# Kernel optimization log

Hardware: AMD Instinct MI355X
Metric: run time of the kernel (lower is better)

The kernel has to match this reference:

```python
import jax, jax.numpy as jnp
import numpy as np

B, T, C = 4, 2048, 768
H, N = 12, 64
N_LAYER, LAYER_ID = 12, 1
EPS_GN = 0.00064


def setup_inputs():
    key = jax.random.key(0)
    ks = jax.random.split(key, 20)
    r01 = LAYER_ID / (N_LAYER - 1)
    r10 = 1.0 - LAYER_ID / N_LAYER
    ddd = (np.arange(C, dtype=np.float64) / C)[None, None, :]

    def lam(p, off=0.0):
        return jnp.asarray(1.0 - np.power(ddd, p) - off, dtype=jnp.float32)

    decay = -7.0 + 5.0 * (np.arange(C, dtype=np.float64) / (C - 1)) ** (0.85 + r01 ** 0.5)

    def rn(i, shape, scale):
        return scale * jax.random.normal(ks[i], shape, jnp.float32)

    s = 1.0 / C ** 0.5
    return {
        "x": jax.random.normal(ks[0], (B, T, C), jnp.float32),
        "v_first": jax.random.normal(ks[1], (B, T, C), jnp.float32),
        "lambda_r": lam(0.2 * r10), "lambda_w": lam(0.9 * r10),
        "lambda_k": lam(0.9 * r10, 0.4 * r01), "lambda_v": lam(0.4 * r10, 0.6 * r01),
        "lambda_a": lam(0.9 * r10), "lambda_g": lam(0.2 * r10),
        "w_miu": jnp.asarray(decay[None, None, :] + 0.5, jnp.float32),
        "w_A": rn(2, (C, 64), 0.02), "w_B": rn(3, (64, C), 0.02),
        "a_miu": jnp.zeros((1, 1, C), jnp.float32),
        "a_A": rn(4, (C, 64), 0.02), "a_B": rn(5, (64, C), 0.02),
        "v_miu": jnp.ones((1, 1, C), jnp.float32),
        "v_A": rn(6, (C, 64), 0.02), "v_B": rn(7, (64, C), 0.02),
        "g_A": rn(8, (C, 128), 0.02), "g_B": rn(9, (128, C), 0.02),
        "k_k": 0.85 * jnp.ones((1, 1, C), jnp.float32),
        "k_a": jnp.ones((1, 1, C), jnp.float32),
        "r_k": rn(10, (H, N), 0.02),
        "W_r": jax.random.uniform(ks[11], (C, C), jnp.float32, -0.5 * s, 0.5 * s),
        "W_k": jax.random.uniform(ks[12], (C, C), jnp.float32, -0.05 * s, 0.05 * s),
        "W_v": jax.random.uniform(ks[13], (C, C), jnp.float32, -0.5 * s, 0.5 * s),
        "W_o": rn(14, (C, C), 0.02),
        "ln_w": jnp.ones((C,), jnp.float32), "ln_b": jnp.zeros((C,), jnp.float32),
    }


def _wkv7(r, w, k, v, z, b):
    # r,w,k,v,z,b: (B,T,H,N). RWKV-7 linear recurrence with per-head NxN state:
    # S_t = S_{t-1}*diag(exp(-exp(w_t))) + (S_{t-1} z_t) b_t^T + v_t k_t^T ; y_t = S_t r_t
    decay = jnp.exp(-jnp.exp(w))

    def step(S, inp):
        rt, dt, kt, vt, zt, bt = inp  # each (B,H,N)
        sa = jnp.einsum('bhij,bhj->bhi', S, zt)
        S = S * dt[:, :, None, :] + sa[..., None] * bt[:, :, None, :] + vt[..., None] * kt[:, :, None, :]
        y = jnp.einsum('bhij,bhj->bhi', S, rt)
        return S, y

    seq = tuple(jnp.moveaxis(t, 1, 0) for t in (r, decay, k, v, z, b))  # (T,B,H,N)
    S0 = jnp.zeros((r.shape[0], r.shape[2], r.shape[3], r.shape[3]), r.dtype)
    _, ys = jax.lax.scan(step, S0, seq)
    return jnp.moveaxis(ys, 0, 1)  # (B,T,H,N)


def reference(x, v_first, lambda_r, lambda_w, lambda_k, lambda_v, lambda_a, lambda_g,
              w_miu, w_A, w_B, a_miu, a_A, a_B, v_miu, v_A, v_B, g_A, g_B,
              k_k, k_a, r_k, W_r, W_k, W_v, W_o, ln_w, ln_b):
    Bb, Tt, Cc = x.shape
    # ZeroPad2d((0,0,1,-1)): shift sequence right by 1, zero at t=0
    x_shift = jnp.pad(x, ((0, 0), (1, 0), (0, 0)))[:, :-1]
    xd = x_shift - x
    r = (x + xd * lambda_r) @ W_r.T
    w = x + xd * lambda_w
    k = (x + xd * lambda_k) @ W_k.T
    v = (x + xd * lambda_v) @ W_v.T
    a_in = x + xd * lambda_a
    g_in = x + xd * lambda_g
    if LAYER_ID == 0:
        v_first = v
    else:
        v = v + (v_first - v) * jax.nn.sigmoid(v_miu + (v @ v_A) @ v_B)
    w = -jax.nn.softplus(-(w_miu + jnp.tanh(w @ w_A) @ w_B)) - 0.5
    a = jax.nn.sigmoid(a_miu + (a_in @ a_A) @ a_B)
    g = jax.nn.sigmoid(g_in @ g_A) @ g_B
    kk = (k * k_k).reshape(Bb, Tt, H, N)
    kk = kk / jnp.maximum(jnp.linalg.norm(kk, axis=-1, keepdims=True), 1e-12)
    k = k * (1 + (a - 1) * k_a)
    rh = r.reshape(Bb, Tt, H, N)
    wh = w.reshape(Bb, Tt, H, N)
    kh = k.reshape(Bb, Tt, H, N)
    vh = v.reshape(Bb, Tt, H, N)
    ah = a.reshape(Bb, Tt, H, N)
    y = _wkv7(rh, wh, kh, vh, -kk, kk * ah)  # (B,T,H,N)
    # GroupNorm over heads, eps=0.00064, biased variance (torch semantics)
    mu = y.mean(-1, keepdims=True)
    var = y.var(-1, keepdims=True)
    y = ((y - mu) / jnp.sqrt(var + EPS_GN)).reshape(Bb, Tt, Cc) * ln_w + ln_b
    y = y + ((rh * kh * r_k).sum(-1, keepdims=True) * vh).reshape(Bb, Tt, Cc)
    out = (y * g) @ W_o.T
    return (out, v_first)
```

## Files before the change

### kernel.cpp

```cpp
#include <hip/hip_runtime.h>
#include <hip/hip_bf16.h>
#include <math.h>


#define B_  4
#define T_  2048
#define C_  768
#define H_  12

typedef __attribute__((ext_vector_type(8))) short bf16x8;
typedef __attribute__((ext_vector_type(4))) float f32x4;

#define GLD16(gsrc, ldst)                                                     \
  __builtin_amdgcn_global_load_lds(                                           \
      (const __attribute__((address_space(1))) void*)(gsrc),                  \
      (__attribute__((address_space(3))) void*)(ldst), 16, 0, 0)

template <int CTRL>
static __device__ __forceinline__ float row_ror_add(float v) {
  int t = __builtin_amdgcn_update_dpp(0, __float_as_int(v), CTRL, 0xF, 0xF, true);
  return v + __int_as_float(t);
}
static __device__ __forceinline__ float row_sum16(float v) {
  v = row_ror_add<0x128>(v);
  v = row_ror_add<0x124>(v);
  v = row_ror_add<0x122>(v);
  v = row_ror_add<0x121>(v);
  return v;
}

static __device__ __forceinline__ float wave_sum64(float v) {
  v = row_sum16(v);
  v += __shfl_xor(v, 16);
  v += __shfl_xor(v, 32);
  return v;
}

static __device__ __forceinline__ short bf16b(float f) {
  __hip_bfloat16 h = __float2bfloat16(f);
  return *reinterpret_cast<short*>(&h);
}

enum { EPI_NONE = 0, EPI_TANH, EPI_WDECAY, EPI_SIGBIAS, EPI_SIGMOID, EPI_VMIX };

static __device__ __forceinline__ float apply_epi_f(int epi, float val, int n,
                                                    int gmrow, int N,
                                                    const float* bias,
                                                    const float* ex1,
                                                    const float* ex2) {
  if (epi == EPI_TANH) {
    val = tanhf(val);
  } else if (epi == EPI_WDECAY) {
    const float u = bias[n] + val;
    const float sig = 1.f / (1.f + expf(-u));
    val = expf(-0.60653065971263342f * sig);
  } else if (epi == EPI_SIGBIAS) {
    const float u = bias[n] + val;
    val = 1.f / (1.f + expf(-u));
  } else if (epi == EPI_SIGMOID) {
    val = 1.f / (1.f + expf(-val));
  } else if (epi == EPI_VMIX) {
    const float u = bias[n] + val;
    const float sg = 1.f / (1.f + expf(-u));
    const size_t off = (size_t)gmrow * N + n;
    const float v0v = ex1[off];
    const float vf = ex2[off];
    val = v0v + (vf - v0v) * sg;
  }
  return val;
}

static __device__ __forceinline__ void gemm128_tile(
    const short* __restrict__ A, const short* __restrict__ Bw,
    float* __restrict__ C, short* __restrict__ C16, int M, int N, int K,
    int bx, int by, int epi, const float* bias, const float* ex1,
    const float* ex2, short* As, short* Bs) {
  const int tid = threadIdx.x;
  const int wave = tid >> 6, lane = tid & 63;
  const int m0 = by * 128, n0 = bx * 128;
  const int wm = (wave >> 1) * 64, wn = (wave & 1) * 64;
  const int fr = lane & 15, fk = (lane >> 4) * 8;

  f32x4 acc[4][4];
#pragma unroll
  for (int i = 0; i < 4; i++)
#pragma unroll
    for (int j = 0; j < 4; j++) acc[i][j] = (f32x4){0.f, 0.f, 0.f, 0.f};

  const int srow = tid >> 2, scol = (tid & 3) * 8;
  const short* gA = A + (size_t)(m0 + srow) * K + scol;
  const short* gB = Bw + (size_t)(n0 + srow) * K + scol;
  short* lA0 = &As[wave * 512];
  short* lA1 = &As[2048 + wave * 512];
  short* lB0 = &Bs[wave * 512];
  short* lB1 = &Bs[2048 + wave * 512];

  for (int k0 = 0; k0 < K; k0 += 32) {
    GLD16(gA + k0, lA0);
    GLD16(gA + (size_t)64 * K + k0, lA1);
    GLD16(gB + k0, lB0);
    GLD16(gB + (size_t)64 * K + k0, lB1);
    __syncthreads();

    bf16x8 af[4], bf[4];
#pragma unroll
    for (int i = 0; i < 4; i++)
      af[i] = *(const bf16x8*)&As[(wm + i * 16 + fr) * 32 + fk];
#pragma unroll
    for (int j = 0; j < 4; j++)
      bf[j] = *(const bf16x8*)&Bs[(wn + j * 16 + fr) * 32 + fk];
#pragma unroll
    for (int i = 0; i < 4; i++)
#pragma unroll
      for (int j = 0; j < 4; j++)
        acc[i][j] =
            __builtin_amdgcn_mfma_f32_16x16x32_bf16(af[i], bf[j], acc[i][j], 0, 0, 0);
    __syncthreads();
  }

#pragma unroll
  for (int i = 0; i < 4; i++) {
    const int gm = m0 + wm + i * 16 + (lane >> 4) * 4;
#pragma unroll
    for (int j = 0; j < 4; j++) {
      const int gn = n0 + wn + j * 16 + fr;
#pragma unroll
      for (int rix = 0; rix < 4; rix++) {
        float val = acc[i][j][rix];
        val = apply_epi_f(epi, val, gn, gm + rix, N, bias, ex1, ex2);
        C[(size_t)(gm + rix) * N + gn] = val;
        if (C16) C16[(size_t)(gm + rix) * N + gn] = bf16b(val);
      }
    }
  }
}

static __device__ __forceinline__ void gemm64_tile(
    const short* __restrict__ A, const short* __restrict__ Bw,
    short* __restrict__ out16, int M, int N, int K, int bx, int by, int epi,
    short* As, short* Bs) {
  const int tid = threadIdx.x;
  const int wave = tid >> 6, lane = tid & 63;
  const int m0 = by * 128, n0 = bx * 64;
  const int wm = (wave >> 1) * 64, wn = (wave & 1) * 32;
  const int fr = lane & 15, fk = (lane >> 4) * 8;

  f32x4 acc[4][2];
#pragma unroll
  for (int i = 0; i < 4; i++)
#pragma unroll
    for (int j = 0; j < 2; j++) acc[i][j] = (f32x4){0.f, 0.f, 0.f, 0.f};

  const int srow = tid >> 2, scol = (tid & 3) * 8;
  const short* gA = A + (size_t)(m0 + srow) * K + scol;
  const short* gB = Bw + (size_t)(n0 + srow) * K + scol;
  short* lA0 = &As[wave * 512];
  short* lA1 = &As[2048 + wave * 512];
  short* lB0 = &Bs[wave * 512];

  for (int k0 = 0; k0 < K; k0 += 32) {
    GLD16(gA + k0, lA0);
    GLD16(gA + (size_t)64 * K + k0, lA1);
    GLD16(gB + k0, lB0);
    __syncthreads();

    bf16x8 af[4], bf[2];
#pragma unroll
    for (int i = 0; i < 4; i++)
      af[i] = *(const bf16x8*)&As[(wm + i * 16 + fr) * 32 + fk];
#pragma unroll
    for (int j = 0; j < 2; j++)
      bf[j] = *(const bf16x8*)&Bs[(wn + j * 16 + fr) * 32 + fk];
#pragma unroll
    for (int i = 0; i < 4; i++)
#pragma unroll
      for (int j = 0; j < 2; j++)
        acc[i][j] =
            __builtin_amdgcn_mfma_f32_16x16x32_bf16(af[i], bf[j], acc[i][j], 0, 0, 0);
    __syncthreads();
  }

#pragma unroll
  for (int i = 0; i < 4; i++) {
    const int gm = m0 + wm + i * 16 + (lane >> 4) * 4;
#pragma unroll
    for (int j = 0; j < 2; j++) {
      const int gn = n0 + wn + j * 16 + fr;
#pragma unroll
      for (int rix = 0; rix < 4; rix++) {
        float val = acc[i][j][rix];
        if (epi == EPI_TANH) val = tanhf(val);
        else if (epi == EPI_SIGMOID) val = 1.f / (1.f + expf(-val));
        out16[(size_t)(gm + rix) * N + gn] = bf16b(val);
      }
    }
  }
}

__global__ __launch_bounds__(256) void big3_k(
    const short* __restrict__ xr, const short* __restrict__ xk,
    const short* __restrict__ xv, const short* __restrict__ wrb,
    const short* __restrict__ wkb, const short* __restrict__ wvb,
    float* __restrict__ r_, float* __restrict__ kbuf,
    float* __restrict__ vbuf, short* __restrict__ vbuf16) {
  __shared__ short smem[2 * 128 * 32];
  const int role = blockIdx.x / 6, bx = blockIdx.x % 6;
  const short* A;
  const short* Bw;
  float* C;
  short* C16 = nullptr;
  if (role == 0) { A = xr; Bw = wrb; C = r_; }
  else if (role == 1) { A = xk; Bw = wkb; C = kbuf; }
  else { A = xv; Bw = wvb; C = vbuf; C16 = vbuf16; }
  gemm128_tile(A, Bw, C, C16, B_ * T_, C_, C_, bx, blockIdx.y, EPI_NONE,
               nullptr, nullptr, nullptr, smem, smem + 128 * 32);
}

__global__ __launch_bounds__(256) void s1x4_k(
    const short* __restrict__ xw, const short* __restrict__ xa,
    const short* __restrict__ xg, const short* __restrict__ vbuf16,
    const short* __restrict__ wAT, const short* __restrict__ aAT,
    const short* __restrict__ gAT, const short* __restrict__ vAT,
    short* __restrict__ h_w, short* __restrict__ h_a,
    short* __restrict__ h_g, short* __restrict__ h_v) {
  __shared__ short smem[128 * 32 + 64 * 32];
  const int bx = blockIdx.x;
  const short* A;
  const short* Bw;
  short* O;
  int N, tb, epi;
  if (bx == 0)      { A = xw;     Bw = wAT; O = h_w; N = 64;  tb = 0; epi = EPI_TANH; }
  else if (bx == 1) { A = xa;     Bw = aAT; O = h_a; N = 64;  tb = 0; epi = EPI_NONE; }
  else if (bx == 2) { A = xg;     Bw = gAT; O = h_g; N = 128; tb = 0; epi = EPI_SIGMOID; }
  else if (bx == 3) { A = xg;     Bw = gAT; O = h_g; N = 128; tb = 1; epi = EPI_SIGMOID; }
  else              { A = vbuf16; Bw = vAT; O = h_v; N = 64;  tb = 0; epi = EPI_NONE; }
  gemm64_tile(A, Bw, O, B_ * T_, N, C_, tb, blockIdx.y, epi, smem,
              smem + 128 * 32);
}

__global__ __launch_bounds__(256) void s2x3_k(
    const short* __restrict__ h_v, const short* __restrict__ h_w,
    const short* __restrict__ h_a, const short* __restrict__ vBT,
    const short* __restrict__ wBT, const short* __restrict__ aBT,
    float* __restrict__ vbuf, float* __restrict__ dec_, float* __restrict__ a_,
    const float* __restrict__ v_miu, const float* __restrict__ w_miu,
    const float* __restrict__ a_miu, const float* __restrict__ v_first) {
  __shared__ short smem[2 * 128 * 32];
  const int role = blockIdx.x / 6, bx = blockIdx.x % 6;
  const short* A;
  const short* Bw;
  float* C;
  const float* bias;
  const float* ex1 = nullptr;
  const float* ex2 = nullptr;
  int epi;
  if (role == 0) { A = h_v; Bw = vBT; C = vbuf; bias = v_miu; ex1 = vbuf; ex2 = v_first; epi = EPI_VMIX; }
  else if (role == 1) { A = h_w; Bw = wBT; C = dec_; bias = w_miu; epi = EPI_WDECAY; }
  else { A = h_a; Bw = aBT; C = a_; bias = a_miu; epi = EPI_SIGBIAS; }
  gemm128_tile(A, Bw, C, nullptr, B_ * T_, C_, 64, bx, blockIdx.y, epi, bias,
               ex1, ex2, smem, smem + 128 * 32);
}

__global__ __launch_bounds__(256) void outp_k(
    const short* __restrict__ ymb, const short* __restrict__ wob,
    float* __restrict__ out) {
  __shared__ short smem[2 * 128 * 32];
  gemm128_tile(ymb, wob, out, nullptr, B_ * T_, C_, C_, blockIdx.x,
               blockIdx.y, EPI_NONE, nullptr, nullptr, nullptr, smem,
               smem + 128 * 32);
}

__global__ __launch_bounds__(256) void mix6_k(
    const float* __restrict__ x, const float* __restrict__ lr,
    const float* __restrict__ lk, const float* __restrict__ lv,
    const float* __restrict__ lw, const float* __restrict__ la,
    const float* __restrict__ lg, short* __restrict__ xr,
    short* __restrict__ xk, short* __restrict__ xv, short* __restrict__ xw,
    short* __restrict__ xa, short* __restrict__ xg) {
  const int i = blockIdx.x * 256 + threadIdx.x;
  const int c4 = i % (C_ / 4);
  const int gm = i / (C_ / 4);
  const float4 xa4 = ((const float4*)x)[i];
  float4 xp = make_float4(0.f, 0.f, 0.f, 0.f);
  if ((gm % T_) != 0) xp = ((const float4*)x)[i - C_ / 4];
  const float4 dx =
      make_float4(xp.x - xa4.x, xp.y - xa4.y, xp.z - xa4.z, xp.w - xa4.w);

#define MIXOUT(dst, lam)                                                      \
  {                                                                           \
    const float4 l4 = ((const float4*)lam)[c4];                               \
    short4 o = {bf16b(fmaf(dx.x, l4.x, xa4.x)),                               \
                bf16b(fmaf(dx.y, l4.y, xa4.y)),                               \
                bf16b(fmaf(dx.z, l4.z, xa4.z)),                               \
                bf16b(fmaf(dx.w, l4.w, xa4.w))};                              \
    ((short4*)dst)[i] = o;                                                    \
  }
  MIXOUT(xr, lr);
  MIXOUT(xk, lk);
  MIXOUT(xv, lv);
  MIXOUT(xw, lw);
  MIXOUT(xa, la);
  MIXOUT(xg, lg);
#undef MIXOUT
}

__global__ __launch_bounds__(256) void wprep_k(
    const float* __restrict__ W_r, const float* __restrict__ W_k,
    const float* __restrict__ W_v, const float* __restrict__ W_o,
    const float* __restrict__ w_A, const float* __restrict__ a_A,
    const float* __restrict__ v_A, const float* __restrict__ g_A,
    const float* __restrict__ w_B, const float* __restrict__ a_B,
    const float* __restrict__ v_B, const float* __restrict__ g_B,
    short* __restrict__ wrb, short* __restrict__ wkb,
    short* __restrict__ wvb, short* __restrict__ wob,
    short* __restrict__ wAT, short* __restrict__ aAT,
    short* __restrict__ vAT, short* __restrict__ gAT,
    short* __restrict__ wBT, short* __restrict__ aBT,
    short* __restrict__ vBT, short* __restrict__ gBT) {
  const int job = blockIdx.y;
  const int WN = C_ * C_;
  if (job < 4) {
    const float* src = (job == 0) ? W_r : (job == 1) ? W_k : (job == 2) ? W_v : W_o;
    short* dst = (job == 0) ? wrb : (job == 1) ? wkb : (job == 2) ? wvb : wob;
    const int n4 = WN / 4;
    for (int i = blockIdx.x * 256 + threadIdx.x; i < n4; i += gridDim.x * 256) {
      const float4 v = ((const float4*)src)[i];
      short4 o = {bf16b(v.x), bf16b(v.y), bf16b(v.z), bf16b(v.w)};
      ((short4*)dst)[i] = o;
    }
  } else {
    const float* in;
    short* out;
    int R, Cc;
    switch (job) {
      case 4: in = w_A; out = wAT; R = C_; Cc = 64; break;
      case 5: in = a_A; out = aAT; R = C_; Cc = 64; break;
      case 6: in = v_A; out = vAT; R = C_; Cc = 64; break;
      case 7: in = g_A; out = gAT; R = C_; Cc = 128; break;
      case 8: in = w_B; out = wBT; R = 64; Cc = C_; break;
      case 9: in = a_B; out = aBT; R = 64; Cc = C_; break;
      case 10: in = v_B; out = vBT; R = 64; Cc = C_; break;
      default: in = g_B; out = gBT; R = 128; Cc = C_; break;
    }
    const int n = R * Cc;
    for (int i = blockIdx.x * 256 + threadIdx.x; i < n; i += gridDim.x * 256) {
      const int r = i / Cc, c = i % Cc;
      out[(size_t)c * R + r] = bf16b(in[i]);
    }
  }
}

__global__ __launch_bounds__(256) void kkprep_k(
    const float* __restrict__ k0, const float* __restrict__ a,
    const float* __restrict__ k_k, const float* __restrict__ k_a,
    float* __restrict__ kout, float* __restrict__ z, float* __restrict__ bb) {
  const int wid = threadIdx.x >> 6;
  const int lane = threadIdx.x & 63;
  const size_t hid = (size_t)blockIdx.x * 4 + wid;
  const int h = (int)(hid % H_);
  const size_t idx = hid * 64 + lane;
  const int c = h * 64 + lane;
  const float kv = k0[idx];
  const float av = a[idx];
  const float kk = kv * k_k[c];
  const float ss = wave_sum64(kk * kk);
  const float denom = fmaxf(sqrtf(ss), 1e-12f);
  const float kkn = kk / denom;
  z[idx] = -kkn;
  bb[idx] = kkn * av;
  kout[idx] = kv * (1.f + (av - 1.f) * k_a[c]);
}

#define CH 16
#define NC (T_ / CH)
__global__ __launch_bounds__(256) void wkv7f_k(
    const float* __restrict__ rr, const float* __restrict__ dd,
    const float* __restrict__ kk, const float* __restrict__ vv,
    const float* __restrict__ zz, const float* __restrict__ bbv,
    float* __restrict__ yy, const short* __restrict__ h_g,
    const short* __restrict__ gBT, float* __restrict__ g_,
    const float4* __restrict__ cpsrc, float4* __restrict__ cpdst, int n4) {
  __shared__ __align__(16) char smem[2 * 5 * CH * 64 * 4];
  const int blk = blockIdx.x;

  if (blk >= 240) {
    const int rb = blk - 240;
    for (int i = rb * 256 + threadIdx.x; i < n4; i += 16 * 256)
      cpdst[i] = cpsrc[i];
    return;
  }
  if (blk >= 192) {
    short* As = (short*)smem;
    short* Bs = As + 128 * 32;
    const int rb = blk - 192;
    for (int it = 0; it < 8; ++it) {
      const int tile = rb + it * 48;
      gemm128_tile(h_g, gBT, g_, nullptr, B_ * T_, C_, 128, tile % 6,
                   tile / 6, EPI_NONE, nullptr, nullptr, nullptr, As, Bs);
    }
    return;
  }

  float* lds = (float*)smem;
  const int bh = blk % 48;
  const int rq = blk / 48;
  const int b = bh / H_, h = bh % H_;
  const int tid = threadIdx.x;
  const int wave = tid >> 6;
  const int l = tid & 63;
  const int l16 = l & 15;
  const int row = rq * 16 + wave * 4 + (l >> 4);
  const int cb = l16 * 4;
  const size_t btb = (size_t)b * T_;

  const size_t g0 = (btb + wave * 4 + (l >> 4)) * C_ + h * 64 + cb;
  const int dbase = wave * 256;
  const size_t vrow0 = btb * C_ + h * 64 + row;

#define STAGE(BUF, GOFF)                                                      \
  {                                                                           \
    float* Ld = lds + (BUF) * 5120;                                           \
    GLD16(dd + (GOFF), Ld + 0 * 1024 + dbase);                                \
    GLD16(zz + (GOFF), Ld + 1 * 1024 + dbase);                                \
    GLD16(bbv + (GOFF), Ld + 2 * 1024 + dbase);                               \
    GLD16(kk + (GOFF), Ld + 3 * 1024 + dbase);                                \
    GLD16(rr + (GOFF), Ld + 4 * 1024 + dbase);                                \
  }

#define LDSTEP(S_, TL_)                                                       \
  {                                                                           \
    Wf[S_] = *(const float4*)&Lb[0 * 1024 + (TL_) * 64 + cb];                 \
    Zf[S_] = *(const float4*)&Lb[1 * 1024 + (TL_) * 64 + cb];                 \
    Bf[S_] = *(const float4*)&Lb[2 * 1024 + (TL_) * 64 + cb];                 \
    Kf[S_] = *(const float4*)&Lb[3 * 1024 + (TL_) * 64 + cb];                 \
    Rf[S_] = *(const float4*)&Lb[4 * 1024 + (TL_) * 64 + cb];                 \
  }

#define PREFV(ARR, CC)                                                        \
  {                                                                           \
    const size_t vb = vrow0 + (size_t)(CC) * CH * C_;                         \
    _Pragma("unroll") for (int j = 0; j < CH; ++j)                            \
        ARR[j] = vv[vb + (size_t)j * C_];                                     \
  }

#define CHUNK_BODY(VARR, CIDX)                                                \
  {                                                                           \
    float4 Wf[3], Zf[3], Bf[3], Kf[3], Rf[3];                                 \
    LDSTEP(0, 0);                                                             \
    LDSTEP(1, 1);                                                             \
    _Pragma("unroll") for (int tl = 0; tl < CH; ++tl) {                       \
      const int sl = tl % 3;                                                  \
      if (tl + 2 < CH) { LDSTEP((tl + 2) % 3, tl + 2); }                      \
      const float4 w4 = Wf[sl], z4 = Zf[sl], b4 = Bf[sl], k4 = Kf[sl],        \
                   r4 = Rf[sl];                                               \
      const float vi = VARR[tl];                                              \
      float sa = fmaf(S1, z4.y, S0 * z4.x) + fmaf(S3, z4.w, S2 * z4.z);       \
      sa = row_sum16(sa);                                                     \
      S0 = fmaf(S0, w4.x, fmaf(sa, b4.x, vi * k4.x));                         \
      S1 = fmaf(S1, w4.y, fmaf(sa, b4.y, vi * k4.y));                         \
      S2 = fmaf(S2, w4.z, fmaf(sa, b4.z, vi * k4.z));                         \
      S3 = fmaf(S3, w4.w, fmaf(sa, b4.w, vi * k4.w));                         \
      float yp = fmaf(S1, r4.y, S0 * r4.x) + fmaf(S3, r4.w, S2 * r4.z);       \
      yp = row_sum16(yp);                                                     \
      if (l16 == 0) yy[ybase + (size_t)((CIDX)*CH + tl) * C_] = yp;           \
    }                                                                         \
  }

  float vA[CH], vB[CH];
  STAGE(0, g0);
  PREFV(vA, 0);
  __syncthreads();

  float S0 = 0.f, S1 = 0.f, S2 = 0.f, S3 = 0.f;
  size_t gpf = g0 + (size_t)CH * C_;
  const size_t ybase = btb * C_ + h * 64 + row;

  for (int c = 0; c < NC; c += 2) {
    PREFV(vB, c + 1);
    STAGE(1, gpf);
    gpf += (size_t)CH * C_;
    {
      const float* Lb = lds;
      CHUNK_BODY(vA, c)
    }
    __syncthreads();
    {
      const int cn = (c + 2 < NC) ? (c + 2) : (NC - 1);
      PREFV(vA, cn);
    }
    if (c + 2 < NC) STAGE(0, gpf);
    gpf += (size_t)CH * C_;
    {
      const float* Lb = lds + 5120;
      CHUNK_BODY(vB, c + 1)
    }
    __syncthreads();
  }
#undef STAGE
#undef LDSTEP
#undef PREFV
#undef CHUNK_BODY
}

__global__ __launch_bounds__(256) void gn_k(
    const float* __restrict__ y, const float* __restrict__ r,
    const float* __restrict__ k, const float* __restrict__ v,
    const float* __restrict__ g, const float* __restrict__ r_k,
    const float* __restrict__ ln_w, const float* __restrict__ ln_b,
    short* __restrict__ ymb) {
  const int wid = threadIdx.x >> 6;
  const int lane = threadIdx.x & 63;
  const size_t hid = (size_t)blockIdx.x * 4 + wid;
  const int h = (int)(hid % H_);
  const size_t idx = hid * 64 + lane;
  const int c = h * 64 + lane;

  const float yv = y[idx];
  const float mu = wave_sum64(yv) * (1.f / 64.f);
  const float sq = wave_sum64(yv * yv) * (1.f / 64.f);
  const float var = sq - mu * mu;
  float yn = (yv - mu) * rsqrtf(var + 0.00064f);
  yn = yn * ln_w[c] + ln_b[c];

  const float s = wave_sum64(r[idx] * k[idx] * r_k[c]);
  yn += s * v[idx];
  ymb[idx] = bf16b(yn * g[idx]);
}

extern "C" void kernel_launch(void* const* d_in, const int* in_sizes, int n_in,
                              void* d_out, int out_size, void* d_ws,
                              size_t ws_size, hipStream_t stream) {
  const float* x       = (const float*)d_in[0];
  const float* v_first = (const float*)d_in[1];
  const float* lam_r   = (const float*)d_in[2];
  const float* lam_w   = (const float*)d_in[3];
  const float* lam_k   = (const float*)d_in[4];
  const float* lam_v   = (const float*)d_in[5];
  const float* lam_a   = (const float*)d_in[6];
  const float* lam_g   = (const float*)d_in[7];
  const float* w_miu   = (const float*)d_in[8];
  const float* w_A     = (const float*)d_in[9];
  const float* w_B     = (const float*)d_in[10];
  const float* a_miu   = (const float*)d_in[11];
  const float* a_A     = (const float*)d_in[12];
  const float* a_B     = (const float*)d_in[13];
  const float* v_miu   = (const float*)d_in[14];
  const float* v_A     = (const float*)d_in[15];
  const float* v_B     = (const float*)d_in[16];
  const float* g_A     = (const float*)d_in[17];
  const float* g_B     = (const float*)d_in[18];
  const float* k_k     = (const float*)d_in[19];
  const float* k_a     = (const float*)d_in[20];
  const float* r_k     = (const float*)d_in[21];
  const float* W_r     = (const float*)d_in[22];
  const float* W_k     = (const float*)d_in[23];
  const float* W_v     = (const float*)d_in[24];
  const float* W_o     = (const float*)d_in[25];
  const float* ln_w    = (const float*)d_in[26];
  const float* ln_b    = (const float*)d_in[27];

  const int M = B_ * T_;
  const size_t S = (size_t)M * C_;

  float* ws   = (float*)d_ws;
  float* r_   = ws + 0 * S;
  float* kbuf = ws + 1 * S;
  float* vbuf = ws + 2 * S;
  float* dec_ = ws + 3 * S;
  float* a_   = ws + 4 * S;
  float* g_   = ws + 5 * S;
  float* z_   = ws + 6 * S;
  float* bb_  = ws + 7 * S;
  float* h_   = ws + 8 * S;
  short* wb   = (short*)(h_ + (size_t)M * 128);
  float* out  = (float*)d_out;

  const int WN = C_ * C_;
  short* wrb = wb + 0 * (size_t)WN;
  short* wkb = wb + 1 * (size_t)WN;
  short* wvb = wb + 2 * (size_t)WN;
  short* wob = wb + 3 * (size_t)WN;
  short* wAT = wb + 4 * (size_t)WN;
  short* aAT = wAT + (size_t)C_ * 64;
  short* vAT = aAT + (size_t)C_ * 64;
  short* gAT = vAT + (size_t)C_ * 64;
  short* wBT = gAT + (size_t)C_ * 128;
  short* aBT = wBT + (size_t)C_ * 64;
  short* vBT = aBT + (size_t)C_ * 64;
  short* gBT = vBT + (size_t)C_ * 64;

  short* xr  = (short*)dec_;
  short* xk  = (short*)a_;
  short* xv  = (short*)g_;
  short* xw  = (short*)z_;
  short* xa  = (short*)z_ + S;
  short* xg  = (short*)bb_;
  short* vbuf16 = (short*)bb_ + S;
  short* h_w = (short*)h_;
  short* h_a = h_w + (size_t)M * 64;
  short* h_g = h_a + (size_t)M * 64;
  short* h_v = (short*)g_;
  short* ymb = (short*)z_;

  {
    dim3 blk(256), grid(576, 12);
    hipLaunchKernelGGL(wprep_k, grid, blk, 0, stream, W_r, W_k, W_v, W_o,
                       w_A, a_A, v_A, g_A, w_B, a_B, v_B, g_B, wrb, wkb, wvb,
                       wob, wAT, aAT, vAT, gAT, wBT, aBT, vBT, gBT);
  }
  {
    dim3 blk(256), grid((int)(S / 4 / 256));
    hipLaunchKernelGGL(mix6_k, grid, blk, 0, stream, x, lam_r, lam_k, lam_v,
                       lam_w, lam_a, lam_g, xr, xk, xv, xw, xa, xg);
  }
  {
    dim3 blk(256), grid(18, M / 128);
    hipLaunchKernelGGL(big3_k, grid, blk, 0, stream, xr, xk, xv, wrb, wkb,
                       wvb, r_, kbuf, vbuf, vbuf16);
  }
  {
    dim3 blk(256), grid(5, M / 128);
    hipLaunchKernelGGL(s1x4_k, grid, blk, 0, stream, xw, xa, xg, vbuf16, wAT,
                       aAT, gAT, vAT, h_w, h_a, h_g, h_v);
  }
  {
    dim3 blk(256), grid(18, M / 128);
    hipLaunchKernelGGL(s2x3_k, grid, blk, 0, stream, h_v, h_w, h_a, vBT, wBT,
                       aBT, vbuf, dec_, a_, v_miu, w_miu, a_miu, v_first);
  }
  {
    dim3 grid((B_ * T_ * H_) / 4), blk(256);
    hipLaunchKernelGGL(kkprep_k, grid, blk, 0, stream, kbuf, a_, k_k, k_a,
                       kbuf, z_, bb_);
  }
  {
    dim3 grid(256), blk(256);
    hipLaunchKernelGGL(wkv7f_k, grid, blk, 0, stream, r_, dec_, kbuf, vbuf,
                       z_, bb_, a_, h_g, gBT, g_, (const float4*)v_first,
                       (float4*)(out + S), (int)(S / 4));
  }
  {
    dim3 grid((B_ * T_ * H_) / 4), blk(256);
    hipLaunchKernelGGL(gn_k, grid, blk, 0, stream, a_, r_, kbuf, vbuf, g_, r_k,
                       ln_w, ln_b, ymb);
  }
  {
    dim3 blk(256), grid(C_ / 128, M / 128);
    hipLaunchKernelGGL(outp_k, grid, blk, 0, stream, ymb, wob, out);
  }
}
```

Baseline: 738.4 us.

## Pack z/b and k/r as bf16 and stage v through LDS in WKV scan

kkprep now writes z with b, and k with r, as interleaved bf16 pairs using vectorized float4 loads and a 16-lane reduction. The recurrence kernel stages decay, v and the two bf16 streams into LDS with async global-to-LDS loads, replacing per-thread strided v prefetches. The aim is to cut the memory traffic and latency of the serial scan's inputs. In exchange z, b, k and r lose precision in the recurrence, which may move accuracy.

```diff
diff --git a/kernel.cpp b/kernel.cpp
--- a/kernel.cpp
+++ b/kernel.cpp
@@ -39,6 +39,11 @@
 static __device__ __forceinline__ short bf16b(float f) {
   __hip_bfloat16 h = __float2bfloat16(f);
   return *reinterpret_cast<short*>(&h);
+}
+
+static __device__ __forceinline__ float bf2f(short s) {
+  const unsigned u = ((unsigned)(unsigned short)s) << 16;
+  return __int_as_float((int)u);
 }
 
 enum { EPI_NONE = 0, EPI_TANH, EPI_WDECAY, EPI_SIGBIAS, EPI_SIGMOID, EPI_VMIX };
@@ -351,36 +356,57 @@
 }
 
 __global__ __launch_bounds__(256) void kkprep_k(
-    const float* __restrict__ k0, const float* __restrict__ a,
-    const float* __restrict__ k_k, const float* __restrict__ k_a,
-    float* __restrict__ kout, float* __restrict__ z, float* __restrict__ bb) {
-  const int wid = threadIdx.x >> 6;
-  const int lane = threadIdx.x & 63;
-  const size_t hid = (size_t)blockIdx.x * 4 + wid;
+    const float* __restrict__ k0, const float* __restrict__ av_,
+    const float* __restrict__ rr, const float* __restrict__ k_k,
+    const float* __restrict__ k_a, float* __restrict__ kout,
+    short* __restrict__ zb16, short* __restrict__ kr16) {
+  const int tid = threadIdx.x;
+  const int wv = tid >> 6, l = tid & 63;
+  const int grp = l >> 4, g16 = l & 15;
+  const size_t hid = (size_t)blockIdx.x * 16 + wv * 4 + grp;
   const int h = (int)(hid % H_);
-  const size_t idx = hid * 64 + lane;
-  const int c = h * 64 + lane;
-  const float kv = k0[idx];
-  const float av = a[idx];
-  const float kk = kv * k_k[c];
-  const float ss = wave_sum64(kk * kk);
+  const size_t base = hid * 64 + g16 * 4;
+  const int cc = h * 64 + g16 * 4;
+
+  const float4 kv = *(const float4*)(k0 + base);
+  const float4 aa = *(const float4*)(av_ + base);
+  const float4 rv = *(const float4*)(rr + base);
+  const float4 kkc = *(const float4*)(k_k + cc);
+  const float4 kac = *(const float4*)(k_a + cc);
+
+  const float kkx = kv.x * kkc.x, kky = kv.y * kkc.y, kkz = kv.z * kkc.z,
+              kkw = kv.w * kkc.w;
+  const float ssp = kkx * kkx + kky * kky + kkz * kkz + kkw * kkw;
+  const float ss = row_sum16(ssp);
   const float denom = fmaxf(sqrtf(ss), 1e-12f);
-  const float kkn = kk / denom;
-  z[idx] = -kkn;
-  bb[idx] = kkn * av;
-  kout[idx] = kv * (1.f + (av - 1.f) * k_a[c]);
+  const float nx = kkx / denom, ny = kky / denom, nz = kkz / denom,
+              nw = kkw / denom;
+
+  bf16x8 zb = {bf16b(-nx), bf16b(-ny), bf16b(-nz), bf16b(-nw),
+               bf16b(nx * aa.x), bf16b(ny * aa.y), bf16b(nz * aa.z),
+               bf16b(nw * aa.w)};
+  *(bf16x8*)(zb16 + hid * 128 + g16 * 8) = zb;
+
+  const float knx = kv.x * (1.f + (aa.x - 1.f) * kac.x);
+  const float kny = kv.y * (1.f + (aa.y - 1.f) * kac.y);
+  const float knz = kv.z * (1.f + (aa.z - 1.f) * kac.z);
+  const float knw = kv.w * (1.f + (aa.w - 1.f) * kac.w);
+  bf16x8 kr = {bf16b(knx), bf16b(kny), bf16b(knz), bf16b(knw),
+               bf16b(rv.x), bf16b(rv.y), bf16b(rv.z), bf16b(rv.w)};
+  *(bf16x8*)(kr16 + hid * 128 + g16 * 8) = kr;
+
+  *(float4*)(kout + base) = make_float4(knx, kny, knz, knw);
 }
 
 #define CH 16
 #define NC (T_ / CH)
 __global__ __launch_bounds__(256) void wkv7f_k(
-    const float* __restrict__ rr, const float* __restrict__ dd,
-    const float* __restrict__ kk, const float* __restrict__ vv,
-    const float* __restrict__ zz, const float* __restrict__ bbv,
+    const float* __restrict__ dd, const float* __restrict__ vv,
+    const short* __restrict__ zb16, const short* __restrict__ kr16,
     float* __restrict__ yy, const short* __restrict__ h_g,
     const short* __restrict__ gBT, float* __restrict__ g_,
     const float4* __restrict__ cpsrc, float4* __restrict__ cpdst, int n4) {
-  __shared__ __align__(16) char smem[2 * 5 * CH * 64 * 4];
+  __shared__ __align__(16) char smem[2 * 16384];
   const int blk = blockIdx.x;
 
   if (blk >= 240) {
@@ -401,7 +427,6 @@
     return;
   }
 
-  float* lds = (float*)smem;
   const int bh = blk % 48;
   const int rq = blk / 48;
   const int b = bh / H_, h = bh % H_;
@@ -413,92 +438,94 @@
   const int cb = l16 * 4;
   const size_t btb = (size_t)b * T_;
 
-  const size_t g0 = (btb + wave * 4 + (l >> 4)) * C_ + h * 64 + cb;
-  const int dbase = wave * 256;
-  const size_t vrow0 = btb * C_ + h * 64 + row;
-
-#define STAGE(BUF, GOFF)                                                      \
+  const size_t gf0 = (btb + wave * 4 + (l >> 4)) * C_ + h * 64 + cb;
+  const size_t gp0 =
+      ((btb + wave * 4 + (l >> 4)) * H_ + h) * 128 + (size_t)(l & 15) * 8;
+
+#define STAGE(BUF, GF, GP)                                                    \
   {                                                                           \
-    float* Ld = lds + (BUF) * 5120;                                           \
-    GLD16(dd + (GOFF), Ld + 0 * 1024 + dbase);                                \
-    GLD16(zz + (GOFF), Ld + 1 * 1024 + dbase);                                \
-    GLD16(bbv + (GOFF), Ld + 2 * 1024 + dbase);                               \
-    GLD16(kk + (GOFF), Ld + 3 * 1024 + dbase);                                \
-    GLD16(rr + (GOFF), Ld + 4 * 1024 + dbase);                                \
+    char* Bb = smem + (BUF)*16384;                                            \
+    GLD16(dd + (GF), (float*)Bb + wave * 256);                                \
+    GLD16(vv + (GF), (float*)(Bb + 4096) + wave * 256);                       \
+    GLD16(zb16 + (GP), (short*)(Bb + 8192) + wave * 512);                     \
+    GLD16(kr16 + (GP), (short*)(Bb + 12288) + wave * 512);                    \
   }
 
 #define LDSTEP(S_, TL_)                                                       \
   {                                                                           \
-    Wf[S_] = *(const float4*)&Lb[0 * 1024 + (TL_) * 64 + cb];                 \
-    Zf[S_] = *(const float4*)&Lb[1 * 1024 + (TL_) * 64 + cb];                 \
-    Bf[S_] = *(const float4*)&Lb[2 * 1024 + (TL_) * 64 + cb];                 \
-    Kf[S_] = *(const float4*)&Lb[3 * 1024 + (TL_) * 64 + cb];                 \
-    Rf[S_] = *(const float4*)&Lb[4 * 1024 + (TL_) * 64 + cb];                 \
-  }
-
-#define PREFV(ARR, CC)                                                        \
+    Wf[S_] = *(const float4*)&Lw[(TL_)*64 + cb];                              \
+    Vf[S_] = Lv[(TL_)*64 + row];                                              \
+    ZB[S_] = *(const bf16x8*)&Lzb[(TL_)*128 + l16 * 8];                       \
+    KR[S_] = *(const bf16x8*)&Lkr[(TL_)*128 + l16 * 8];                       \
+  }
+
+#define CHUNK_BODY(CIDX)                                                      \
   {                                                                           \
-    const size_t vb = vrow0 + (size_t)(CC) * CH * C_;                         \
-    _Pragma("unroll") for (int j = 0; j < CH; ++j)                            \
-        ARR[j] = vv[vb + (size_t)j * C_];                                     \
-  }
-
-#define CHUNK_BODY(VARR, CIDX)                                                \
-  {                                                                           \
-    float4 Wf[3], Zf[3], Bf[3], Kf[3], Rf[3];                                 \
+    float4 Wf[3];                                                             \
+    float Vf[3];                                                              \
+    bf16x8 ZB[3], KR[3];                                                      \
     LDSTEP(0, 0);                                                             \
     LDSTEP(1, 1);                                                             \
     _Pragma("unroll") for (int tl = 0; tl < CH; ++tl) {                       \
       const int sl = tl % 3;                                                  \
       if (tl + 2 < CH) { LDSTEP((tl + 2) % 3, tl + 2); }                      \
-      const float4 w4 = Wf[sl], z4 = Zf[sl], b4 = Bf[sl], k4 = Kf[sl],        \
-                   r4 = Rf[sl];                                               \
-      const float vi = VARR[tl];                                              \
-      float sa = fmaf(S1, z4.y, S0 * z4.x) + fmaf(S3, z4.w, S2 * z4.z);       \
+      const float4 w4 = Wf[sl];                                               \
+      const float vi = Vf[sl];                                                \
+      const bf16x8 zb = ZB[sl], kr = KR[sl];                                  \
+      const float z0 = bf2f(zb[0]), z1 = bf2f(zb[1]), z2 = bf2f(zb[2]),       \
+                  z3 = bf2f(zb[3]);                                           \
+      const float b0 = bf2f(zb[4]), b1 = bf2f(zb[5]), b2 = bf2f(zb[6]),       \
+                  b3 = bf2f(zb[7]);                                           \
+      const float k0 = bf2f(kr[0]), k1 = bf2f(kr[1]), k2 = bf2f(kr[2]),       \
+                  k3 = bf2f(kr[3]);                                           \
+      const float r0 = bf2f(kr[4]), r1 = bf2f(kr[5]), r2 = bf2f(kr[6]),       \
+                  r3 = bf2f(kr[7]);                                           \
+      float sa = fmaf(S1, z1, S0 * z0) + fmaf(S3, z3, S2 * z2);               \
       sa = row_sum16(sa);                                                     \
-      S0 = fmaf(S0, w4.x, fmaf(sa, b4.x, vi * k4.x));                         \
-      S1 = fmaf(S1, w4.y, fmaf(sa, b4.y, vi * k4.y));                         \
-      S2 = fmaf(S2, w4.z, fmaf(sa, b4.z, vi * k4.z));                         \
-      S3 = fmaf(S3, w4.w, fmaf(sa, b4.w, vi * k4.w));                         \
-      float yp = fmaf(S1, r4.y, S0 * r4.x) + fmaf(S3, r4.w, S2 * r4.z);       \
+      S0 = fmaf(S0, w4.x, fmaf(sa, b0, vi * k0));                             \
+      S1 = fmaf(S1, w4.y, fmaf(sa, b1, vi * k1));                             \
+      S2 = fmaf(S2, w4.z, fmaf(sa, b2, vi * k2));                             \
+      S3 = fmaf(S3, w4.w, fmaf(sa, b3, vi * k3));                             \
+      float yp = fmaf(S1, r1, S0 * r0) + fmaf(S3, r3, S2 * r2);               \
       yp = row_sum16(yp);                                                     \
       if (l16 == 0) yy[ybase + (size_t)((CIDX)*CH + tl) * C_] = yp;           \
     }                                                                         \
   }
 
-  float vA[CH], vB[CH];
-  STAGE(0, g0);
-  PREFV(vA, 0);
+  STAGE(0, gf0, gp0);
   __syncthreads();
 
   float S0 = 0.f, S1 = 0.f, S2 = 0.f, S3 = 0.f;
-  size_t gpf = g0 + (size_t)CH * C_;
+  size_t gf = gf0 + (size_t)CH * C_;
+  size_t gp = gp0 + (size_t)CH * H_ * 128;
   const size_t ybase = btb * C_ + h * 64 + row;
 
   for (int c = 0; c < NC; c += 2) {
-    PREFV(vB, c + 1);
-    STAGE(1, gpf);
-    gpf += (size_t)CH * C_;
+    STAGE(1, gf, gp);
+    gf += (size_t)CH * C_;
+    gp += (size_t)CH * H_ * 128;
     {
-      const float* Lb = lds;
-      CHUNK_BODY(vA, c)
+      const float* Lw = (const float*)(smem);
+      const float* Lv = (const float*)(smem + 4096);
+      const short* Lzb = (const short*)(smem + 8192);
+      const short* Lkr = (const short*)(smem + 12288);
+      CHUNK_BODY(c)
     }
     __syncthreads();
+    if (c + 2 < NC) STAGE(0, gf, gp);
+    gf += (size_t)CH * C_;
+    gp += (size_t)CH * H_ * 128;
     {
-      const int cn = (c + 2 < NC) ? (c + 2) : (NC - 1);
-      PREFV(vA, cn);
-    }
-    if (c + 2 < NC) STAGE(0, gpf);
-    gpf += (size_t)CH * C_;
-    {
-      const float* Lb = lds + 5120;
-      CHUNK_BODY(vB, c + 1)
+      const float* Lw = (const float*)(smem + 16384);
+      const float* Lv = (const float*)(smem + 16384 + 4096);
+      const short* Lzb = (const short*)(smem + 16384 + 8192);
+      const short* Lkr = (const short*)(smem + 16384 + 12288);
+      CHUNK_BODY(c + 1)
     }
     __syncthreads();
   }
 #undef STAGE
 #undef LDSTEP
-#undef PREFV
 #undef CHUNK_BODY
 }
 
@@ -600,6 +627,8 @@
   short* h_a = h_w + (size_t)M * 64;
   short* h_g = h_a + (size_t)M * 64;
   short* h_v = (short*)g_;
+  short* zb16 = (short*)z_;
+  short* kr16 = (short*)bb_;
   short* ymb = (short*)z_;
 
   {
@@ -629,14 +658,14 @@
                        aBT, vbuf, dec_, a_, v_miu, w_miu, a_miu, v_first);
   }
   {
-    dim3 grid((B_ * T_ * H_) / 4), blk(256);
-    hipLaunchKernelGGL(kkprep_k, grid, blk, 0, stream, kbuf, a_, k_k, k_a,
-                       kbuf, z_, bb_);
+    dim3 grid((B_ * T_ * H_) / 16), blk(256);
+    hipLaunchKernelGGL(kkprep_k, grid, blk, 0, stream, kbuf, a_, r_, k_k,
+                       k_a, kbuf, zb16, kr16);
   }
   {
     dim3 grid(256), blk(256);
-    hipLaunchKernelGGL(wkv7f_k, grid, blk, 0, stream, r_, dec_, kbuf, vbuf,
-                       z_, bb_, a_, h_g, gBT, g_, (const float4*)v_first,
+    hipLaunchKernelGGL(wkv7f_k, grid, blk, 0, stream, dec_, vbuf, zb16, kr16,
+                       a_, h_g, gBT, g_, (const float4*)v_first,
                        (float4*)(out + S), (int)(S / 4));
   }
   {
```

Result: no change. 741.0 us (+0.3%).
